# Kernel optimization log

Hardware: AMD Instinct MI355X
Metric: run time of the kernel (lower is better)

The kernel has to match this reference:

```python
import jax, jax.numpy as jnp
import numpy as np

H = 2048   # hidden_size
L = 512    # latent_dim
B, S = 4, 2048

def setup_inputs() -> dict:
    key = jax.random.key(0)
    ks = jax.random.split(key, 13)
    def lin(k, fan_in, shape):
        bound = 1.0 / np.sqrt(fan_in)
        return jax.random.uniform(k, shape, jnp.float32, -bound, bound)
    return {
        "hidden_states": jax.random.normal(ks[0], (B, S, H), jnp.float32),
        "num_reasoning_steps": 8,
        # to_latent: Linear(H, 2L) -> ReLU -> Linear(2L, L)
        "W_enc1": lin(ks[1], H, (2 * L, H)), "b_enc1": lin(ks[2], H, (2 * L,)),
        "W_enc2": lin(ks[3], 2 * L, (L, 2 * L)), "b_enc2": lin(ks[4], 2 * L, (L,)),
        # from_latent: Linear(L, 2L) -> ReLU -> Linear(2L, H)
        "W_dec1": lin(ks[5], L, (2 * L, L)), "b_dec1": lin(ks[6], L, (2 * L,)),
        "W_dec2": lin(ks[7], 2 * L, (H, 2 * L)), "b_dec2": lin(ks[8], 2 * L, (H,)),
        # GRUCell(L, L): weight_ih/hh [3L, L], bias_ih/hh [3L]
        "w_ih": lin(ks[9], L, (3 * L, L)), "w_hh": lin(ks[10], L, (3 * L, L)),
        "b_ih": lin(ks[11], L, (3 * L,)), "b_hh": lin(ks[12], L, (3 * L,)),
    }

def _gru_cell(x, h, w_ih, w_hh, b_ih, b_hh):
    # PyTorch GRUCell semantics
    gi = x @ w_ih.T + b_ih   # [*, 3L]
    gh = h @ w_hh.T + b_hh
    i_r, i_z, i_n = jnp.split(gi, 3, axis=-1)
    h_r, h_z, h_n = jnp.split(gh, 3, axis=-1)
    r = jax.nn.sigmoid(i_r + h_r)
    z = jax.nn.sigmoid(i_z + h_z)
    n = jnp.tanh(i_n + r * h_n)
    return (1.0 - z) * n + z * h

def reference(hidden_states, num_reasoning_steps, W_enc1, b_enc1, W_enc2, b_enc2,
              W_dec1, b_dec1, W_dec2, b_dec2, w_ih, w_hh, b_ih, b_hh):
    # encode to latent
    latent = jax.nn.relu(hidden_states @ W_enc1.T + b_enc1) @ W_enc2.T + b_enc2  # [B,S,L]

    def step(lat, _):
        lat = _gru_cell(lat, lat, w_ih, w_hh, b_ih, b_hh)
        return lat, lat

    latent, traj = jax.lax.scan(step, latent, None, length=num_reasoning_steps)
    # traj: [steps, B, S, L] -> [B, S, steps, L]
    latent_trajectory = jnp.transpose(traj, (1, 2, 0, 3))
    decoded = jax.nn.relu(latent @ W_dec1.T + b_dec1) @ W_dec2.T + b_dec2  # [B,S,H]
    return decoded, latent_trajectory
```

## Files before the change

### kernel.cpp

```cpp
#include <hip/hip_runtime.h>
#include <hip/hip_bf16.h>
#include <cstdint>
#include <cstddef>

#define TOKENS   8192
#define HID      2048
#define LAT      512
#define LAT2     1024
#define GCOLS    2048
#define STEPS    8
#define DEC_ELEMS (TOKENS*HID)

typedef __attribute__((ext_vector_type(8))) __bf16 bf16x8;
typedef __attribute__((ext_vector_type(4))) float  f32x4;
typedef __attribute__((ext_vector_type(8))) unsigned short u16x8;

__device__ __forceinline__ unsigned short f32_to_bf16_rne(float f) {
  unsigned int u = __float_as_uint(f);
  unsigned int r = (u + 0x7FFFu + ((u >> 16) & 1u)) >> 16;
  return (unsigned short)r;
}
__device__ __forceinline__ float bf16_to_f32(unsigned short u) {
  return __uint_as_float(((unsigned int)u) << 16);
}

__device__ __forceinline__ float sigmoidf_(float x) {
  if (x >= 0.f) { float e = __expf(-x); return 1.f / (1.f + e); }
  float e = __expf(x); return e / (1.f + e);
}
__device__ __forceinline__ float tanhf_(float x) {
  float ax = fabsf(x);
  float e  = __expf(-2.f * ax);
  float t  = (1.f - e) / (1.f + e);
  return copysignf(t, x);
}

__device__ __forceinline__ void gl_lds16(const void* g, void* l) {
  __builtin_amdgcn_global_load_lds(
      (const __attribute__((address_space(1))) void*)g,
      (__attribute__((address_space(3))) void*)l, 16, 0, 0);
}

__global__ void k_prep_w(const float* __restrict__ We1, const float* __restrict__ We2,
                         const float* __restrict__ Wd1, const float* __restrict__ Wd2,
                         unsigned short* __restrict__ We1b, unsigned short* __restrict__ We2b,
                         unsigned short* __restrict__ Wd1b, unsigned short* __restrict__ Wd2b) {
  const int total = 1310720;
  int i = blockIdx.x * blockDim.x + threadIdx.x;
  int stride = gridDim.x * blockDim.x;
  for (; i < total; i += stride) {
    const float* s; unsigned short* d; int j;
    if (i < 524288)       { s = We1; d = We1b; j = i; }
    else if (i < 655360)  { s = We2; d = We2b; j = i - 524288; }
    else if (i < 786432)  { s = Wd1; d = Wd1b; j = i - 655360; }
    else                  { s = Wd2; d = Wd2b; j = i - 786432; }
    float4 v = ((const float4*)s)[j];
    ushort4 o;
    o.x = f32_to_bf16_rne(v.x);
    o.y = f32_to_bf16_rne(v.y);
    o.z = f32_to_bf16_rne(v.z);
    o.w = f32_to_bf16_rne(v.w);
    ((ushort4*)d)[j] = o;
  }
}

__global__ void k_gru_pack(const float* __restrict__ wih, const float* __restrict__ whh,
                           const float* __restrict__ bih, const float* __restrict__ bhh,
                           unsigned short* __restrict__ Wg, float* __restrict__ biasg) {
  int gc = blockIdx.x;
  int l  = gc >> 2;
  int g  = gc & 3;
  int row = (g == 0) ? l : (g == 1) ? (512 + l) : (1024 + l);
  for (int c = threadIdx.x; c < LAT; c += blockDim.x) {
    float v;
    if (g <= 1)      v = wih[row * LAT + c] + whh[row * LAT + c];
    else if (g == 2) v = wih[row * LAT + c];
    else             v = whh[row * LAT + c];
    Wg[(size_t)gc * LAT + c] = f32_to_bf16_rne(v);
  }
  if (threadIdx.x == 0) {
    float b;
    if (g <= 1)      b = bih[row] + bhh[row];
    else if (g == 2) b = bih[row];
    else             b = bhh[row];
    biasg[gc] = b;
  }
}

#define MWG 128
#define NWG 128
#define KTILE 64

template <int EPI, int A32>
__global__ __launch_bounds__(256)
void gemm_bt(const void* __restrict__ Ap,
             const unsigned short* __restrict__ W,
             const float* __restrict__ bias,
             int K, int N,
             unsigned short* __restrict__ outB) {
  __shared__ __align__(16) char smem[2 * MWG * KTILE * 2];
  unsigned short* As = (unsigned short*)smem;
  unsigned short* Bs = As + MWG * KTILE;

  const int tid  = threadIdx.x;
  const int lane = tid & 63;
  const int wv   = tid >> 6;
  const int wr   = wv >> 1;
  const int wc   = wv & 1;
  const int m0   = blockIdx.x * MWG;
  const int n0   = blockIdx.y * NWG;

  const int lr = lane & 15;
  const int lq = lane >> 4;
  const int srow = lane >> 3;
  const int scol = (lane & 7) * 8;

  f32x4 acc[4][4];
#pragma unroll
  for (int i = 0; i < 4; ++i)
#pragma unroll
    for (int j = 0; j < 4; ++j) acc[i][j] = (f32x4){0.f, 0.f, 0.f, 0.f};

  const unsigned short* Ab = (const unsigned short*)Ap + (size_t)m0 * K;
  const float*          Af = (const float*)Ap + (size_t)m0 * K;
  const unsigned short* Wb = W + (size_t)n0 * K;

  const int KT = K / KTILE;
  for (int kt = 0; kt < KT; ++kt) {
    const int k0 = kt * KTILE;
#pragma unroll
    for (int q = 0; q < 4; ++q) {
      int row = 32 * wv + 8 * q + srow;
      if constexpr (!A32)
        gl_lds16(Ab + (size_t)row * K + k0 + scol, As + (32 * wv + 8 * q) * KTILE);
      gl_lds16(Wb + (size_t)row * K + k0 + scol, Bs + (32 * wv + 8 * q) * KTILE);
    }
    if constexpr (A32) {
#pragma unroll
      for (int q = 0; q < 4; ++q) {
        int row = 32 * wv + 8 * q + srow;
        const float* src = Af + (size_t)row * K + k0 + scol;
        float4 v0 = *(const float4*)src;
        float4 v1 = *(const float4*)(src + 4);
        u16x8 o;
        o[0] = f32_to_bf16_rne(v0.x); o[1] = f32_to_bf16_rne(v0.y);
        o[2] = f32_to_bf16_rne(v0.z); o[3] = f32_to_bf16_rne(v0.w);
        o[4] = f32_to_bf16_rne(v1.x); o[5] = f32_to_bf16_rne(v1.y);
        o[6] = f32_to_bf16_rne(v1.z); o[7] = f32_to_bf16_rne(v1.w);
        *(u16x8*)(As + (32 * wv + 8 * q) * KTILE + lane * 8) = o;
      }
    }
    __syncthreads();
#pragma unroll
    for (int kk = 0; kk < KTILE; kk += 32) {
      bf16x8 af[4], bf[4];
#pragma unroll
      for (int i = 0; i < 4; ++i)
        af[i] = *(const bf16x8*)(As + (wr * 64 + i * 16 + lr) * KTILE + kk + lq * 8);
#pragma unroll
      for (int j = 0; j < 4; ++j)
        bf[j] = *(const bf16x8*)(Bs + (wc * 64 + j * 16 + lr) * KTILE + kk + lq * 8);
#pragma unroll
      for (int i = 0; i < 4; ++i)
#pragma unroll
        for (int j = 0; j < 4; ++j)
          acc[i][j] = __builtin_amdgcn_mfma_f32_16x16x32_bf16(af[i], bf[j], acc[i][j], 0, 0, 0);
    }
    __syncthreads();
  }

  float bj[4];
#pragma unroll
  for (int j = 0; j < 4; ++j) bj[j] = bias[n0 + wc * 64 + j * 16 + lr];
#pragma unroll
  for (int i = 0; i < 4; ++i) {
#pragma unroll
    for (int ii = 0; ii < 4; ++ii) {
      int row = m0 + wr * 64 + i * 16 + 4 * lq + ii;
#pragma unroll
      for (int j = 0; j < 4; ++j) {
        int col = n0 + wc * 64 + j * 16 + lr;
        float v = acc[i][j][ii] + bj[j];
        if constexpr (EPI == 0) {
          outB[(size_t)row * N + col] = f32_to_bf16_rne(fmaxf(v, 0.f));
        } else {
          outB[(size_t)row * N + col] = f32_to_bf16_rne(v);
        }
      }
    }
  }
}


#define WAIT_LGKM0() asm volatile("s_waitcnt lgkmcnt(0)" ::: "memory")
#define WAIT_VM(n)   asm volatile("s_waitcnt vmcnt(" #n ")" ::: "memory")

#define LOAD_A(buf, mh) { \
  const int baseA = (buf)*65536 + wm*16384; \
  _Pragma("unroll") for (int m4 = 0; m4 < 4; ++m4) \
  _Pragma("unroll") for (int kki = 0; kki < 2; ++kki) { \
    int rl = (mh)*64 + m4*16 + lr; \
    int off = (rl*128 + kki*64 + lq*16) ^ ((rl & 7) << 4); \
    aR[mh][m4][kki] = *(const bf16x8*)(lds_ + baseA + off); } }

#define LOAD_B(buf, nh) { \
  const int baseB = (buf)*65536 + 32768 + (wn >> 1)*16384; \
  _Pragma("unroll") for (int n2 = 0; n2 < 2; ++n2) \
  _Pragma("unroll") for (int kki = 0; kki < 2; ++kki) { \
    int rl = (wn & 1)*64 + ((nh)*2 + n2)*16 + lr; \
    int off = (rl*128 + kki*64 + lq*16) ^ ((rl & 7) << 4); \
    bR[nh][n2][kki] = *(const bf16x8*)(lds_ + baseB + off); } }

#define STAGE_A(buf, half, kt) { \
  const unsigned short* gp = A + (size_t)(m0 + (half)*128 + rr8)*K + (size_t)(kt)*64 + cc8; \
  char* dp = lds_ + (buf)*65536 + (half)*16384 + (wv << 10); \
  gl_lds16(gp, dp); \
  gl_lds16(gp + (size_t)64*K, dp + 8192); }

#define STAGE_B(buf, half, kt) { \
  const unsigned short* gp = W + (size_t)(n0 + (half)*128 + rr8)*K + (size_t)(kt)*64 + cc8; \
  char* dp = lds_ + (buf)*65536 + 32768 + (half)*16384 + (wv << 10); \
  gl_lds16(gp, dp); \
  gl_lds16(gp + (size_t)64*K, dp + 8192); }

#define MFMAQ(mh, nh) \
  _Pragma("unroll") for (int kki = 0; kki < 2; ++kki) \
  _Pragma("unroll") for (int n2 = 0; n2 < 2; ++n2) \
  _Pragma("unroll") for (int m4 = 0; m4 < 4; ++m4) \
    acc[(mh)*4 + m4][(nh)*2 + n2] = __builtin_amdgcn_mfma_f32_16x16x32_bf16( \
        aR[mh][m4][kki], bR[nh][n2][kki], acc[(mh)*4 + m4][(nh)*2 + n2], 0, 0, 0);

#define PH_CORE(mh, nh) \
  __builtin_amdgcn_s_barrier(); \
  WAIT_LGKM0(); \
  __builtin_amdgcn_sched_barrier(0); \
  __builtin_amdgcn_s_setprio(1); \
  MFMAQ(mh, nh); \
  __builtin_amdgcn_sched_barrier(0); \
  __builtin_amdgcn_s_setprio(0);

#define PH_BAR() __builtin_amdgcn_s_barrier();

#define KLOOP_MAIN(tlim) \
  _Pragma("unroll 1") \
  for (int t = 0; t < (tlim); ++t) { \
    const int kt1 = 2 * t + 1, kt2 = 2 * t + 2, kt3 = 2 * t + 3; \
    LOAD_A(0, 0) LOAD_B(0, 0) \
    STAGE_A(1, 0, kt1) \
    PH_CORE(0, 0) PH_BAR() \
    LOAD_B(0, 1) \
    STAGE_A(1, 1, kt1) \
    PH_CORE(0, 1) PH_BAR() \
    LOAD_A(0, 1) \
    STAGE_B(0, 0, kt2) \
    PH_CORE(1, 1) PH_BAR() \
    STAGE_B(0, 1, kt2) \
    PH_CORE(1, 0) \
    WAIT_VM(4); \
    PH_BAR() \
    LOAD_A(1, 0) LOAD_B(1, 0) \
    STAGE_A(0, 0, kt2) \
    PH_CORE(0, 0) PH_BAR() \
    LOAD_B(1, 1) \
    STAGE_A(0, 1, kt2) \
    PH_CORE(0, 1) PH_BAR() \
    LOAD_A(1, 1) \
    STAGE_B(1, 0, kt3) \
    PH_CORE(1, 1) PH_BAR() \
    STAGE_B(1, 1, kt3) \
    PH_CORE(1, 0) \
    WAIT_VM(4); \
    PH_BAR() \
  }

#define KLOOP_LAST(ktL) { \
    LOAD_A(0, 0) LOAD_B(0, 0) \
    STAGE_A(1, 0, (ktL)) \
    PH_CORE(0, 0) PH_BAR() \
    LOAD_B(0, 1) \
    STAGE_A(1, 1, (ktL)) \
    PH_CORE(0, 1) PH_BAR() \
    LOAD_A(0, 1) \
    PH_CORE(1, 1) PH_BAR() \
    PH_CORE(1, 0) \
    WAIT_VM(0); \
    PH_BAR() \
    LOAD_A(1, 0) LOAD_B(1, 0) \
    PH_CORE(0, 0) PH_BAR() \
    LOAD_B(1, 1) \
    PH_CORE(0, 1) PH_BAR() \
    LOAD_A(1, 1) \
    PH_CORE(1, 1) PH_BAR() \
    PH_CORE(1, 0) \
    PH_BAR() \
  }

__global__ __launch_bounds__(512, 2)
void gemm256_f(const unsigned short* __restrict__ A,
               const unsigned short* __restrict__ W,
               const float* __restrict__ bias, int K, int N, int Ntiles,
               float* __restrict__ outF) {
  __shared__ __align__(16) char lds_[131072];

  const int tid  = threadIdx.x;
  const int lane = tid & 63;
  const int wv   = tid >> 6;
  const int wm   = wv >> 2;
  const int wn   = wv & 3;
  const int lr   = lane & 15;
  const int lq   = lane >> 4;
  const int rr8 = (wv << 3) + (lane >> 3);
  const int cc8 = ((lane & 7) ^ (lane >> 3)) << 3;

  const int nwg = gridDim.x;
  const int wg  = blockIdx.x;
  const int swz = (wg & 7) * (nwg >> 3) + (wg >> 3);
  const int tm  = swz / Ntiles;
  const int tn  = swz % Ntiles;
  const int m0  = tm * 256;
  const int n0  = tn * 256;

  f32x4 acc[8][4];
#pragma unroll
  for (int i = 0; i < 8; ++i)
#pragma unroll
    for (int j = 0; j < 4; ++j) acc[i][j] = (f32x4){0.f, 0.f, 0.f, 0.f};

  bf16x8 aR[2][4][2];
  bf16x8 bR[2][2][2];

  const int nIt = K >> 7;

  STAGE_B(0, 0, 0) STAGE_B(0, 1, 0) STAGE_A(0, 0, 0) STAGE_A(0, 1, 0)
  STAGE_B(1, 0, 1) STAGE_B(1, 1, 1)
  WAIT_VM(4);
  __builtin_amdgcn_s_barrier();

  KLOOP_MAIN(nIt - 1)
  KLOOP_LAST(2 * nIt - 1)

  float bj[4];
#pragma unroll
  for (int nf = 0; nf < 4; ++nf) bj[nf] = bias[n0 + wn * 64 + nf * 16 + lr];
#pragma unroll
  for (int mf = 0; mf < 8; ++mf) {
#pragma unroll
    for (int ii = 0; ii < 4; ++ii) {
      int row = m0 + wm * 128 + mf * 16 + lq * 4 + ii;
#pragma unroll
      for (int nf = 0; nf < 4; ++nf) {
        int col = n0 + wn * 64 + nf * 16 + lr;
        outF[(size_t)row * N + col] = acc[mf][nf][ii] + bj[nf];
      }
    }
  }
}

__global__ __launch_bounds__(512, 2)
void gemm256_gru(const unsigned short* __restrict__ A,
                 const unsigned short* __restrict__ W,
                 const float* __restrict__ bias,
                 int K, int N, int Ntiles,
                 unsigned short* __restrict__ outB,
                 const unsigned short* __restrict__ hInB,
                 float* __restrict__ traj,
                 int step) {
  __shared__ __align__(16) char lds_[131072];

  const int tid  = threadIdx.x;
  const int lane = tid & 63;
  const int wv   = tid >> 6;
  const int wm   = wv >> 2;
  const int wn   = wv & 3;
  const int lr   = lane & 15;
  const int lq   = lane >> 4;
  const int rr8 = (wv << 3) + (lane >> 3);
  const int cc8 = ((lane & 7) ^ (lane >> 3)) << 3;

  const int nwg = gridDim.x;
  const int wg  = blockIdx.x;
  const int swz = (wg & 7) * (nwg >> 3) + (wg >> 3);
  const int tm  = swz / Ntiles;
  const int tn  = swz % Ntiles;
  const int m0  = tm * 256;
  const int n0  = tn * 256;

  f32x4 acc[8][4];
#pragma unroll
  for (int i = 0; i < 8; ++i)
#pragma unroll
    for (int j = 0; j < 4; ++j) acc[i][j] = (f32x4){0.f, 0.f, 0.f, 0.f};

  bf16x8 aR[2][4][2];
  bf16x8 bR[2][2][2];

  const int nIt = K >> 7;

  STAGE_B(0, 0, 0) STAGE_B(0, 1, 0) STAGE_A(0, 0, 0) STAGE_A(0, 1, 0)
  STAGE_B(1, 0, 1) STAGE_B(1, 1, 1)
  WAIT_VM(4);
  __builtin_amdgcn_s_barrier();

  KLOOP_MAIN(nIt - 1)
  KLOOP_LAST(2 * nIt - 1)

  float bj[4];
#pragma unroll
  for (int nf = 0; nf < 4; ++nf) bj[nf] = bias[n0 + wn * 64 + nf * 16 + lr];

  float* scr = (float*)lds_ + wv * 1088;
  const int latBase = tn * 64 + wn * 16;
  const int la = lane & 15;
  const int th = lane >> 4;
#pragma unroll
  for (int mf = 0; mf < 8; ++mf) {
    WAIT_LGKM0();
#pragma unroll
    for (int nf = 0; nf < 4; ++nf)
#pragma unroll
      for (int ii = 0; ii < 4; ++ii)
        scr[(lq * 4 + ii) * 68 + nf * 16 + lr] = acc[mf][nf][ii] + bj[nf];
    WAIT_LGKM0();
#pragma unroll
    for (int tb = 0; tb < 4; ++tb) {
      int tt = th * 4 + tb;
      int token = m0 + wm * 128 + mf * 16 + tt;
      f32x4 g = *(const f32x4*)(scr + tt * 68 + la * 4);
      int latc = latBase + la;
      float h  = bf16_to_f32(hInB[(size_t)token * LAT + latc]);
      float r  = sigmoidf_(g.x);
      float z  = sigmoidf_(g.y);
      float n  = tanhf_(g.z + r * g.w);
      float hn = (1.f - z) * n + z * h;
      outB[(size_t)token * LAT + latc] = f32_to_bf16_rne(hn);
      traj[(size_t)token * (STEPS * LAT) + step * LAT + latc] = hn;
    }
  }
}

extern "C" void kernel_launch(void* const* d_in, const int* in_sizes, int n_in,
                              void* d_out, int out_size, void* d_ws, size_t ws_size,
                              hipStream_t stream) {
  const float* hs  = (const float*)d_in[0];
  const float* We1 = (const float*)d_in[2];
  const float* be1 = (const float*)d_in[3];
  const float* We2 = (const float*)d_in[4];
  const float* be2 = (const float*)d_in[5];
  const float* Wd1 = (const float*)d_in[6];
  const float* bd1 = (const float*)d_in[7];
  const float* Wd2 = (const float*)d_in[8];
  const float* bd2 = (const float*)d_in[9];
  const float* wih = (const float*)d_in[10];
  const float* whh = (const float*)d_in[11];
  const float* bih = (const float*)d_in[12];
  const float* bhh = (const float*)d_in[13];

  char* ws = (char*)d_ws;
  unsigned short* X2    = (unsigned short*)(ws + 0);
  unsigned short* We1b  = (unsigned short*)(ws + 33554432);
  unsigned short* We2b  = (unsigned short*)(ws + 37748736);
  unsigned short* Wd1b  = (unsigned short*)(ws + 38797312);
  unsigned short* Wd2b  = (unsigned short*)(ws + 39845888);
  unsigned short* Wg    = (unsigned short*)(ws + 44040192);
  float*          biasg = (float*)         (ws + 46137344);
  unsigned short* X1    = (unsigned short*)(ws + 46145536);
  unsigned short* Lb0   = (unsigned short*)(ws + 62922752);
  unsigned short* Lb1   = (unsigned short*)(ws + 71311360);

  float* dec  = (float*)d_out;
  float* traj = (float*)d_out + DEC_ELEMS;

  k_prep_w<<<1024, 256, 0, stream>>>(We1, We2, Wd1, Wd2, We1b, We2b, Wd1b, Wd2b);
  k_gru_pack<<<GCOLS, 128, 0, stream>>>(wih, whh, bih, bhh, Wg, biasg);

  gemm_bt<0, 1><<<dim3(TOKENS / MWG, LAT2 / NWG), dim3(256), 0, stream>>>(
      hs, We1b, be1, HID, LAT2, X1);
  gemm_bt<1, 0><<<dim3(TOKENS / MWG, LAT / NWG), dim3(256), 0, stream>>>(
      X1, We2b, be2, LAT2, LAT, Lb0);
  for (int s = 0; s < STEPS; ++s) {
    const unsigned short* lbi = (s & 1) ? Lb1 : Lb0;
    unsigned short*       lbo = (s & 1) ? Lb0 : Lb1;
    gemm256_gru<<<256, 512, 0, stream>>>(lbi, Wg, biasg, LAT, GCOLS, 8,
                                         lbo, lbi, traj, s);
  }
  gemm_bt<0, 0><<<dim3(TOKENS / MWG, LAT2 / NWG), dim3(256), 0, stream>>>(
      Lb0, Wd1b, bd1, LAT, LAT2, X2);
  gemm256_f<<<256, 512, 0, stream>>>(X2, Wd2b, bd2, LAT2, HID, 8, dec);
}
```

Baseline: 441.5 us.

## Run GRU steps on 128x128 gemm_bt tiles and merge weight-prep kernels

Replaces the 256x256 pipelined GRU GEMM with a new epilogue mode (EPI=2) of the simpler 128x128 gemm_bt kernel. This launches four times as many workgroups per step, spreading the short-K GEMM more evenly across CUs. The two weight-prep kernels are also merged into one launch to save a dispatch. The trade-off is that the GRU path loses the deeper LDS pipelining and the larger per-block data reuse of the 256-tile kernel.

Result: slower. 477.5 us (+8.2%).

```diff
diff --git a/kernel.cpp b/kernel.cpp
--- a/kernel.cpp
+++ b/kernel.cpp
@@ -41,49 +41,55 @@
       (__attribute__((address_space(3))) void*)l, 16, 0, 0);
 }
 
-__global__ void k_prep_w(const float* __restrict__ We1, const float* __restrict__ We2,
-                         const float* __restrict__ Wd1, const float* __restrict__ Wd2,
-                         unsigned short* __restrict__ We1b, unsigned short* __restrict__ We2b,
-                         unsigned short* __restrict__ Wd1b, unsigned short* __restrict__ Wd2b) {
-  const int total = 1310720;
-  int i = blockIdx.x * blockDim.x + threadIdx.x;
-  int stride = gridDim.x * blockDim.x;
-  for (; i < total; i += stride) {
-    const float* s; unsigned short* d; int j;
-    if (i < 524288)       { s = We1; d = We1b; j = i; }
-    else if (i < 655360)  { s = We2; d = We2b; j = i - 524288; }
-    else if (i < 786432)  { s = Wd1; d = Wd1b; j = i - 655360; }
-    else                  { s = Wd2; d = Wd2b; j = i - 786432; }
-    float4 v = ((const float4*)s)[j];
-    ushort4 o;
-    o.x = f32_to_bf16_rne(v.x);
-    o.y = f32_to_bf16_rne(v.y);
-    o.z = f32_to_bf16_rne(v.z);
-    o.w = f32_to_bf16_rne(v.w);
-    ((ushort4*)d)[j] = o;
-  }
-}
-
-__global__ void k_gru_pack(const float* __restrict__ wih, const float* __restrict__ whh,
-                           const float* __restrict__ bih, const float* __restrict__ bhh,
-                           unsigned short* __restrict__ Wg, float* __restrict__ biasg) {
-  int gc = blockIdx.x;
-  int l  = gc >> 2;
-  int g  = gc & 3;
-  int row = (g == 0) ? l : (g == 1) ? (512 + l) : (1024 + l);
-  for (int c = threadIdx.x; c < LAT; c += blockDim.x) {
-    float v;
-    if (g <= 1)      v = wih[row * LAT + c] + whh[row * LAT + c];
-    else if (g == 2) v = wih[row * LAT + c];
-    else             v = whh[row * LAT + c];
-    Wg[(size_t)gc * LAT + c] = f32_to_bf16_rne(v);
-  }
-  if (threadIdx.x == 0) {
-    float b;
-    if (g <= 1)      b = bih[row] + bhh[row];
-    else if (g == 2) b = bih[row];
-    else             b = bhh[row];
-    biasg[gc] = b;
+#define WAIT_LGKM0() asm volatile("s_waitcnt lgkmcnt(0)" ::: "memory")
+#define WAIT_VM(n)   asm volatile("s_waitcnt vmcnt(" #n ")" ::: "memory")
+
+__global__ __launch_bounds__(256)
+void k_prep_all(const float* __restrict__ We1, const float* __restrict__ We2,
+                const float* __restrict__ Wd1, const float* __restrict__ Wd2,
+                const float* __restrict__ wih, const float* __restrict__ whh,
+                const float* __restrict__ bih, const float* __restrict__ bhh,
+                unsigned short* __restrict__ We1b, unsigned short* __restrict__ We2b,
+                unsigned short* __restrict__ Wd1b, unsigned short* __restrict__ Wd2b,
+                unsigned short* __restrict__ Wg,   float* __restrict__ biasg) {
+  const int bid = blockIdx.x;
+  if (bid < 2048) {
+    int gc = bid;
+    int l  = gc >> 2;
+    int g  = gc & 3;
+    int row = (g == 0) ? l : (g == 1) ? (512 + l) : (1024 + l);
+    for (int c = threadIdx.x; c < LAT; c += blockDim.x) {
+      float v;
+      if (g <= 1)      v = wih[row * LAT + c] + whh[row * LAT + c];
+      else if (g == 2) v = wih[row * LAT + c];
+      else             v = whh[row * LAT + c];
+      Wg[(size_t)gc * LAT + c] = f32_to_bf16_rne(v);
+    }
+    if (threadIdx.x == 0) {
+      float b;
+      if (g <= 1)      b = bih[row] + bhh[row];
+      else if (g == 2) b = bih[row];
+      else             b = bhh[row];
+      biasg[gc] = b;
+    }
+  } else {
+    const int total = 1310720;
+    int i = (bid - 2048) * blockDim.x + threadIdx.x;
+    int stride = 256 * blockDim.x;
+    for (; i < total; i += stride) {
+      const float* s; unsigned short* d; int j;
+      if (i < 524288)       { s = We1; d = We1b; j = i; }
+      else if (i < 655360)  { s = We2; d = We2b; j = i - 524288; }
+      else if (i < 786432)  { s = Wd1; d = Wd1b; j = i - 655360; }
+      else                  { s = Wd2; d = Wd2b; j = i - 786432; }
+      float4 v = ((const float4*)s)[j];
+      ushort4 o;
+      o.x = f32_to_bf16_rne(v.x);
+      o.y = f32_to_bf16_rne(v.y);
+      o.z = f32_to_bf16_rne(v.z);
+      o.w = f32_to_bf16_rne(v.w);
+      ((ushort4*)d)[j] = o;
+    }
   }
 }
 
@@ -97,7 +103,10 @@
              const unsigned short* __restrict__ W,
              const float* __restrict__ bias,
              int K, int N,
-             unsigned short* __restrict__ outB) {
+             unsigned short* __restrict__ outB,
+             const unsigned short* __restrict__ hInB,
+             float* __restrict__ traj,
+             int step) {
   __shared__ __align__(16) char smem[2 * MWG * KTILE * 2];
   unsigned short* As = (unsigned short*)smem;
   unsigned short* Bs = As + MWG * KTILE;
@@ -172,28 +181,57 @@
   float bj[4];
 #pragma unroll
   for (int j = 0; j < 4; ++j) bj[j] = bias[n0 + wc * 64 + j * 16 + lr];
-#pragma unroll
-  for (int i = 0; i < 4; ++i) {
-#pragma unroll
-    for (int ii = 0; ii < 4; ++ii) {
-      int row = m0 + wr * 64 + i * 16 + 4 * lq + ii;
-#pragma unroll
-      for (int j = 0; j < 4; ++j) {
-        int col = n0 + wc * 64 + j * 16 + lr;
-        float v = acc[i][j][ii] + bj[j];
-        if constexpr (EPI == 0) {
-          outB[(size_t)row * N + col] = f32_to_bf16_rne(fmaxf(v, 0.f));
-        } else {
-          outB[(size_t)row * N + col] = f32_to_bf16_rne(v);
+
+  if constexpr (EPI == 0 || EPI == 1) {
+#pragma unroll
+    for (int i = 0; i < 4; ++i) {
+#pragma unroll
+      for (int ii = 0; ii < 4; ++ii) {
+        int row = m0 + wr * 64 + i * 16 + 4 * lq + ii;
+#pragma unroll
+        for (int j = 0; j < 4; ++j) {
+          int col = n0 + wc * 64 + j * 16 + lr;
+          float v = acc[i][j][ii] + bj[j];
+          if constexpr (EPI == 0) {
+            outB[(size_t)row * N + col] = f32_to_bf16_rne(fmaxf(v, 0.f));
+          } else {
+            outB[(size_t)row * N + col] = f32_to_bf16_rne(v);
+          }
         }
       }
     }
-  }
-}
-
-
-#define WAIT_LGKM0() asm volatile("s_waitcnt lgkmcnt(0)" ::: "memory")
-#define WAIT_VM(n)   asm volatile("s_waitcnt vmcnt(" #n ")" ::: "memory")
+  } else {
+    float* scr = (float*)smem + wv * 1088;
+    const int latBase = (n0 + wc * 64) >> 2;
+    const int la = lane & 15;
+    const int th = lane >> 4;
+#pragma unroll
+    for (int i = 0; i < 4; ++i) {
+      WAIT_LGKM0();
+#pragma unroll
+      for (int j = 0; j < 4; ++j)
+#pragma unroll
+        for (int ii = 0; ii < 4; ++ii)
+          scr[(lq * 4 + ii) * 68 + j * 16 + lr] = acc[i][j][ii] + bj[j];
+      WAIT_LGKM0();
+#pragma unroll
+      for (int tb = 0; tb < 4; ++tb) {
+        int tt = th * 4 + tb;
+        int token = m0 + wr * 64 + i * 16 + tt;
+        f32x4 g = *(const f32x4*)(scr + tt * 68 + la * 4);
+        int latc = latBase + la;
+        float h  = bf16_to_f32(hInB[(size_t)token * LAT + latc]);
+        float r  = sigmoidf_(g.x);
+        float z  = sigmoidf_(g.y);
+        float n  = tanhf_(g.z + r * g.w);
+        float hn = (1.f - z) * n + z * h;
+        outB[(size_t)token * LAT + latc] = f32_to_bf16_rne(hn);
+        traj[(size_t)token * (STEPS * LAT) + step * LAT + latc] = hn;
+      }
+    }
+  }
+}
+
 
 #define LOAD_A(buf, mh) { \
   const int baseA = (buf)*65536 + wm*16384; \
@@ -356,88 +394,6 @@
   }
 }
 
-__global__ __launch_bounds__(512, 2)
-void gemm256_gru(const unsigned short* __restrict__ A,
-                 const unsigned short* __restrict__ W,
-                 const float* __restrict__ bias,
-                 int K, int N, int Ntiles,
-                 unsigned short* __restrict__ outB,
-                 const unsigned short* __restrict__ hInB,
-                 float* __restrict__ traj,
-                 int step) {
-  __shared__ __align__(16) char lds_[131072];
-
-  const int tid  = threadIdx.x;
-  const int lane = tid & 63;
-  const int wv   = tid >> 6;
-  const int wm   = wv >> 2;
-  const int wn   = wv & 3;
-  const int lr   = lane & 15;
-  const int lq   = lane >> 4;
-  const int rr8 = (wv << 3) + (lane >> 3);
-  const int cc8 = ((lane & 7) ^ (lane >> 3)) << 3;
-
-  const int nwg = gridDim.x;
-  const int wg  = blockIdx.x;
-  const int swz = (wg & 7) * (nwg >> 3) + (wg >> 3);
-  const int tm  = swz / Ntiles;
-  const int tn  = swz % Ntiles;
-  const int m0  = tm * 256;
-  const int n0  = tn * 256;
-
-  f32x4 acc[8][4];
-#pragma unroll
-  for (int i = 0; i < 8; ++i)
-#pragma unroll
-    for (int j = 0; j < 4; ++j) acc[i][j] = (f32x4){0.f, 0.f, 0.f, 0.f};
-
-  bf16x8 aR[2][4][2];
-  bf16x8 bR[2][2][2];
-
-  const int nIt = K >> 7;
-
-  STAGE_B(0, 0, 0) STAGE_B(0, 1, 0) STAGE_A(0, 0, 0) STAGE_A(0, 1, 0)
-  STAGE_B(1, 0, 1) STAGE_B(1, 1, 1)
-  WAIT_VM(4);
-  __builtin_amdgcn_s_barrier();
-
-  KLOOP_MAIN(nIt - 1)
-  KLOOP_LAST(2 * nIt - 1)
-
-  float bj[4];
-#pragma unroll
-  for (int nf = 0; nf < 4; ++nf) bj[nf] = bias[n0 + wn * 64 + nf * 16 + lr];
-
-  float* scr = (float*)lds_ + wv * 1088;
-  const int latBase = tn * 64 + wn * 16;
-  const int la = lane & 15;
-  const int th = lane >> 4;
-#pragma unroll
-  for (int mf = 0; mf < 8; ++mf) {
-    WAIT_LGKM0();
-#pragma unroll
-    for (int nf = 0; nf < 4; ++nf)
-#pragma unroll
-      for (int ii = 0; ii < 4; ++ii)
-        scr[(lq * 4 + ii) * 68 + nf * 16 + lr] = acc[mf][nf][ii] + bj[nf];
-    WAIT_LGKM0();
-#pragma unroll
-    for (int tb = 0; tb < 4; ++tb) {
-      int tt = th * 4 + tb;
-      int token = m0 + wm * 128 + mf * 16 + tt;
-      f32x4 g = *(const f32x4*)(scr + tt * 68 + la * 4);
-      int latc = latBase + la;
-      float h  = bf16_to_f32(hInB[(size_t)token * LAT + latc]);
-      float r  = sigmoidf_(g.x);
-      float z  = sigmoidf_(g.y);
-      float n  = tanhf_(g.z + r * g.w);
-      float hn = (1.f - z) * n + z * h;
-      outB[(size_t)token * LAT + latc] = f32_to_bf16_rne(hn);
-      traj[(size_t)token * (STEPS * LAT) + step * LAT + latc] = hn;
-    }
-  }
-}
-
 extern "C" void kernel_launch(void* const* d_in, const int* in_sizes, int n_in,
                               void* d_out, int out_size, void* d_ws, size_t ws_size,
                               hipStream_t stream) {
@@ -470,20 +426,20 @@
   float* dec  = (float*)d_out;
   float* traj = (float*)d_out + DEC_ELEMS;
 
-  k_prep_w<<<1024, 256, 0, stream>>>(We1, We2, Wd1, Wd2, We1b, We2b, Wd1b, Wd2b);
-  k_gru_pack<<<GCOLS, 128, 0, stream>>>(wih, whh, bih, bhh, Wg, biasg);
+  k_prep_all<<<2304, 256, 0, stream>>>(We1, We2, Wd1, Wd2, wih, whh, bih, bhh,
+                                       We1b, We2b, Wd1b, Wd2b, Wg, biasg);
 
   gemm_bt<0, 1><<<dim3(TOKENS / MWG, LAT2 / NWG), dim3(256), 0, stream>>>(
-      hs, We1b, be1, HID, LAT2, X1);
+      hs, We1b, be1, HID, LAT2, X1, nullptr, nullptr, 0);
   gemm_bt<1, 0><<<dim3(TOKENS / MWG, LAT / NWG), dim3(256), 0, stream>>>(
-      X1, We2b, be2, LAT2, LAT, Lb0);
+      X1, We2b, be2, LAT2, LAT, Lb0, nullptr, nullptr, 0);
   for (int s = 0; s < STEPS; ++s) {
     const unsigned short* lbi = (s & 1) ? Lb1 : Lb0;
     unsigned short*       lbo = (s & 1) ? Lb0 : Lb1;
-    gemm256_gru<<<256, 512, 0, stream>>>(lbi, Wg, biasg, LAT, GCOLS, 8,
-                                         lbo, lbi, traj, s);
+    gemm_bt<2, 0><<<dim3(TOKENS / MWG, GCOLS / NWG), dim3(256), 0, stream>>>(
+        lbi, Wg, biasg, LAT, GCOLS, lbo, lbi, traj, s);
   }
   gemm_bt<0, 0><<<dim3(TOKENS / MWG, LAT2 / NWG), dim3(256), 0, stream>>>(
-      Lb0, Wd1b, bd1, LAT, LAT2, X2);
+      Lb0, Wd1b, bd1, LAT, LAT2, X2, nullptr, nullptr, 0);
   gemm256_f<<<256, 512, 0, stream>>>(X2, Wd2b, bd2, LAT2, HID, 8, dec);
 }
```

## Fold GRU and decoder weight prep into first encoder GEMM as extra blocks

Applied to the files above, without the earlier changes.

Only the encoder weight conversion now runs before the first GEMM. The GRU weight packing and decoder weight conversion move into an extra row of blocks (blockIdx.y==8) inside the first encoder GEMM launch, so they overlap with the GEMM and one kernel launch goes away. The GRU pack is also vectorised to float4 loads. The trade-off is 64 extra blocks that compete with the GEMM for compute units and memory bandwidth, which could lengthen its tail.

Result: slower. 461.3 us (+4.5%).

```diff
diff --git a/kernel.cpp b/kernel.cpp
--- a/kernel.cpp
+++ b/kernel.cpp
@@ -41,19 +41,19 @@
       (__attribute__((address_space(3))) void*)l, 16, 0, 0);
 }
 
-__global__ void k_prep_w(const float* __restrict__ We1, const float* __restrict__ We2,
-                         const float* __restrict__ Wd1, const float* __restrict__ Wd2,
-                         unsigned short* __restrict__ We1b, unsigned short* __restrict__ We2b,
-                         unsigned short* __restrict__ Wd1b, unsigned short* __restrict__ Wd2b) {
-  const int total = 1310720;
+#define WAIT_LGKM0() asm volatile("s_waitcnt lgkmcnt(0)" ::: "memory")
+#define WAIT_VM(n)   asm volatile("s_waitcnt vmcnt(" #n ")" ::: "memory")
+
+__global__ __launch_bounds__(256)
+void k_prep_early(const float* __restrict__ We1, const float* __restrict__ We2,
+                  unsigned short* __restrict__ We1b, unsigned short* __restrict__ We2b) {
+  const int total = 655360;
   int i = blockIdx.x * blockDim.x + threadIdx.x;
   int stride = gridDim.x * blockDim.x;
   for (; i < total; i += stride) {
     const float* s; unsigned short* d; int j;
-    if (i < 524288)       { s = We1; d = We1b; j = i; }
-    else if (i < 655360)  { s = We2; d = We2b; j = i - 524288; }
-    else if (i < 786432)  { s = Wd1; d = Wd1b; j = i - 655360; }
-    else                  { s = Wd2; d = Wd2b; j = i - 786432; }
+    if (i < 524288) { s = We1; d = We1b; j = i; }
+    else            { s = We2; d = We2b; j = i - 524288; }
     float4 v = ((const float4*)s)[j];
     ushort4 o;
     o.x = f32_to_bf16_rne(v.x);
@@ -64,26 +64,48 @@
   }
 }
 
-__global__ void k_gru_pack(const float* __restrict__ wih, const float* __restrict__ whh,
-                           const float* __restrict__ bih, const float* __restrict__ bhh,
-                           unsigned short* __restrict__ Wg, float* __restrict__ biasg) {
-  int gc = blockIdx.x;
-  int l  = gc >> 2;
-  int g  = gc & 3;
-  int row = (g == 0) ? l : (g == 1) ? (512 + l) : (1024 + l);
-  for (int c = threadIdx.x; c < LAT; c += blockDim.x) {
-    float v;
-    if (g <= 1)      v = wih[row * LAT + c] + whh[row * LAT + c];
-    else if (g == 2) v = wih[row * LAT + c];
-    else             v = whh[row * LAT + c];
-    Wg[(size_t)gc * LAT + c] = f32_to_bf16_rne(v);
-  }
-  if (threadIdx.x == 0) {
-    float b;
-    if (g <= 1)      b = bih[row] + bhh[row];
-    else if (g == 2) b = bih[row];
-    else             b = bhh[row];
+__device__ void prep_tail(int bx, int tid,
+                          const float* __restrict__ wih, const float* __restrict__ whh,
+                          const float* __restrict__ bih, const float* __restrict__ bhh,
+                          const float* __restrict__ Wd1, const float* __restrict__ Wd2,
+                          unsigned short* __restrict__ Wg, float* __restrict__ biasg,
+                          unsigned short* __restrict__ Wd1b, unsigned short* __restrict__ Wd2b) {
+  const int gtid = bx * 256 + tid;
+  for (int i = gtid; i < 262144; i += 16384) {
+    int gc = i >> 7;
+    int c4 = (i & 127) << 2;
+    int l = gc >> 2, g = gc & 3;
+    int row = (g == 0) ? l : (g == 1) ? (512 + l) : (1024 + l);
+    float4 a = *(const float4*)(wih + (size_t)row * 512 + c4);
+    float4 b = *(const float4*)(whh + (size_t)row * 512 + c4);
+    float4 v;
+    if (g <= 1)      { v.x = a.x + b.x; v.y = a.y + b.y; v.z = a.z + b.z; v.w = a.w + b.w; }
+    else if (g == 2) v = a;
+    else             v = b;
+    ushort4 o;
+    o.x = f32_to_bf16_rne(v.x);
+    o.y = f32_to_bf16_rne(v.y);
+    o.z = f32_to_bf16_rne(v.z);
+    o.w = f32_to_bf16_rne(v.w);
+    *(ushort4*)(Wg + (size_t)gc * 512 + c4) = o;
+  }
+  for (int gc = gtid; gc < 2048; gc += 16384) {
+    int l = gc >> 2, g = gc & 3;
+    int row = (g == 0) ? l : (g == 1) ? (512 + l) : (1024 + l);
+    float b = (g <= 1) ? (bih[row] + bhh[row]) : (g == 2 ? bih[row] : bhh[row]);
     biasg[gc] = b;
+  }
+  for (int i = gtid; i < 655360; i += 16384) {
+    const float* s; unsigned short* d; int j;
+    if (i < 131072) { s = Wd1; d = Wd1b; j = i; }
+    else            { s = Wd2; d = Wd2b; j = i - 131072; }
+    float4 v = ((const float4*)s)[j];
+    ushort4 o;
+    o.x = f32_to_bf16_rne(v.x);
+    o.y = f32_to_bf16_rne(v.y);
+    o.z = f32_to_bf16_rne(v.z);
+    o.w = f32_to_bf16_rne(v.w);
+    ((ushort4*)d)[j] = o;
   }
 }
 
@@ -91,13 +113,26 @@
 #define NWG 128
 #define KTILE 64
 
-template <int EPI, int A32>
+template <int EPI, int A32, int PREP>
 __global__ __launch_bounds__(256)
 void gemm_bt(const void* __restrict__ Ap,
              const unsigned short* __restrict__ W,
              const float* __restrict__ bias,
              int K, int N,
-             unsigned short* __restrict__ outB) {
+             unsigned short* __restrict__ outB,
+             const float* __restrict__ p_wih, const float* __restrict__ p_whh,
+             const float* __restrict__ p_bih, const float* __restrict__ p_bhh,
+             const float* __restrict__ p_Wd1, const float* __restrict__ p_Wd2,
+             unsigned short* __restrict__ p_Wg, float* __restrict__ p_biasg,
+             unsigned short* __restrict__ p_Wd1b, unsigned short* __restrict__ p_Wd2b) {
+  if constexpr (PREP) {
+    if (blockIdx.y == 8) {
+      prep_tail(blockIdx.x, threadIdx.x, p_wih, p_whh, p_bih, p_bhh,
+                p_Wd1, p_Wd2, p_Wg, p_biasg, p_Wd1b, p_Wd2b);
+      return;
+    }
+  }
+
   __shared__ __align__(16) char smem[2 * MWG * KTILE * 2];
   unsigned short* As = (unsigned short*)smem;
   unsigned short* Bs = As + MWG * KTILE;
@@ -191,9 +226,6 @@
   }
 }
 
-
-#define WAIT_LGKM0() asm volatile("s_waitcnt lgkmcnt(0)" ::: "memory")
-#define WAIT_VM(n)   asm volatile("s_waitcnt vmcnt(" #n ")" ::: "memory")
 
 #define LOAD_A(buf, mh) { \
   const int baseA = (buf)*65536 + wm*16384; \
@@ -470,20 +502,22 @@
   float* dec  = (float*)d_out;
   float* traj = (float*)d_out + DEC_ELEMS;
 
-  k_prep_w<<<1024, 256, 0, stream>>>(We1, We2, Wd1, Wd2, We1b, We2b, Wd1b, Wd2b);
-  k_gru_pack<<<GCOLS, 128, 0, stream>>>(wih, whh, bih, bhh, Wg, biasg);
-
-  gemm_bt<0, 1><<<dim3(TOKENS / MWG, LAT2 / NWG), dim3(256), 0, stream>>>(
-      hs, We1b, be1, HID, LAT2, X1);
-  gemm_bt<1, 0><<<dim3(TOKENS / MWG, LAT / NWG), dim3(256), 0, stream>>>(
-      X1, We2b, be2, LAT2, LAT, Lb0);
+  k_prep_early<<<1024, 256, 0, stream>>>(We1, We2, We1b, We2b);
+
+  gemm_bt<0, 1, 1><<<dim3(TOKENS / MWG, 9), dim3(256), 0, stream>>>(
+      hs, We1b, be1, HID, LAT2, X1,
+      wih, whh, bih, bhh, Wd1, Wd2, Wg, biasg, Wd1b, Wd2b);
+  gemm_bt<1, 0, 0><<<dim3(TOKENS / MWG, LAT / NWG), dim3(256), 0, stream>>>(
+      X1, We2b, be2, LAT2, LAT, Lb0,
+      nullptr, nullptr, nullptr, nullptr, nullptr, nullptr, nullptr, nullptr, nullptr, nullptr);
   for (int s = 0; s < STEPS; ++s) {
     const unsigned short* lbi = (s & 1) ? Lb1 : Lb0;
     unsigned short*       lbo = (s & 1) ? Lb0 : Lb1;
     gemm256_gru<<<256, 512, 0, stream>>>(lbi, Wg, biasg, LAT, GCOLS, 8,
                                          lbo, lbi, traj, s);
   }
-  gemm_bt<0, 0><<<dim3(TOKENS / MWG, LAT2 / NWG), dim3(256), 0, stream>>>(
-      Lb0, Wd1b, bd1, LAT, LAT2, X2);
+  gemm_bt<0, 0, 0><<<dim3(TOKENS / MWG, LAT2 / NWG), dim3(256), 0, stream>>>(
+      Lb0, Wd1b, bd1, LAT, LAT2, X2,
+      nullptr, nullptr, nullptr, nullptr, nullptr, nullptr, nullptr, nullptr, nullptr, nullptr);
   gemm256_f<<<256, 512, 0, stream>>>(X2, Wd2b, bd2, LAT2, HID, 8, dec);
 }
```

## Route encoder/decoder GEMMs through pipelined 256-tile kernel and fuse prep kernels

Applied to the files above, without the earlier changes.

Replaces the simple 128x128 gemm_bt kernel used for the two encoder GEMMs and the first decoder GEMM with the templated 256-tile pipelined gemm256 kernel, which gains bf16/ReLU epilogue variants. The fp32 hidden-state input is now converted to bf16 in a merged prep kernel that also converts the weights and packs the GRU weights. Previously that conversion happened inside the first GEMM's load path. This trades an extra 64MB read plus 32MB write for a faster main loop. The encoder GEMMs launch only 128 and 64 workgroups, which may underfill the GPU.

New measurement: 465.7 us. 5.5% more time.

```diff
diff --git a/kernel.cpp b/kernel.cpp
--- a/kernel.cpp
+++ b/kernel.cpp
@@ -13,7 +13,6 @@
 
 typedef __attribute__((ext_vector_type(8))) __bf16 bf16x8;
 typedef __attribute__((ext_vector_type(4))) float  f32x4;
-typedef __attribute__((ext_vector_type(8))) unsigned short u16x8;
 
 __device__ __forceinline__ unsigned short f32_to_bf16_rne(float f) {
   unsigned int u = __float_as_uint(f);
@@ -41,159 +40,64 @@
       (__attribute__((address_space(3))) void*)l, 16, 0, 0);
 }
 
-__global__ void k_prep_w(const float* __restrict__ We1, const float* __restrict__ We2,
-                         const float* __restrict__ Wd1, const float* __restrict__ Wd2,
-                         unsigned short* __restrict__ We1b, unsigned short* __restrict__ We2b,
-                         unsigned short* __restrict__ Wd1b, unsigned short* __restrict__ Wd2b) {
-  const int total = 1310720;
-  int i = blockIdx.x * blockDim.x + threadIdx.x;
-  int stride = gridDim.x * blockDim.x;
-  for (; i < total; i += stride) {
-    const float* s; unsigned short* d; int j;
-    if (i < 524288)       { s = We1; d = We1b; j = i; }
-    else if (i < 655360)  { s = We2; d = We2b; j = i - 524288; }
-    else if (i < 786432)  { s = Wd1; d = Wd1b; j = i - 655360; }
-    else                  { s = Wd2; d = Wd2b; j = i - 786432; }
-    float4 v = ((const float4*)s)[j];
-    ushort4 o;
-    o.x = f32_to_bf16_rne(v.x);
-    o.y = f32_to_bf16_rne(v.y);
-    o.z = f32_to_bf16_rne(v.z);
-    o.w = f32_to_bf16_rne(v.w);
-    ((ushort4*)d)[j] = o;
-  }
-}
-
-__global__ void k_gru_pack(const float* __restrict__ wih, const float* __restrict__ whh,
-                           const float* __restrict__ bih, const float* __restrict__ bhh,
-                           unsigned short* __restrict__ Wg, float* __restrict__ biasg) {
-  int gc = blockIdx.x;
-  int l  = gc >> 2;
-  int g  = gc & 3;
-  int row = (g == 0) ? l : (g == 1) ? (512 + l) : (1024 + l);
-  for (int c = threadIdx.x; c < LAT; c += blockDim.x) {
-    float v;
-    if (g <= 1)      v = wih[row * LAT + c] + whh[row * LAT + c];
-    else if (g == 2) v = wih[row * LAT + c];
-    else             v = whh[row * LAT + c];
-    Wg[(size_t)gc * LAT + c] = f32_to_bf16_rne(v);
-  }
-  if (threadIdx.x == 0) {
-    float b;
-    if (g <= 1)      b = bih[row] + bhh[row];
-    else if (g == 2) b = bih[row];
-    else             b = bhh[row];
-    biasg[gc] = b;
-  }
-}
-
-#define MWG 128
-#define NWG 128
-#define KTILE 64
-
-template <int EPI, int A32>
-__global__ __launch_bounds__(256)
-void gemm_bt(const void* __restrict__ Ap,
-             const unsigned short* __restrict__ W,
-             const float* __restrict__ bias,
-             int K, int N,
-             unsigned short* __restrict__ outB) {
-  __shared__ __align__(16) char smem[2 * MWG * KTILE * 2];
-  unsigned short* As = (unsigned short*)smem;
-  unsigned short* Bs = As + MWG * KTILE;
-
-  const int tid  = threadIdx.x;
-  const int lane = tid & 63;
-  const int wv   = tid >> 6;
-  const int wr   = wv >> 1;
-  const int wc   = wv & 1;
-  const int m0   = blockIdx.x * MWG;
-  const int n0   = blockIdx.y * NWG;
-
-  const int lr = lane & 15;
-  const int lq = lane >> 4;
-  const int srow = lane >> 3;
-  const int scol = (lane & 7) * 8;
-
-  f32x4 acc[4][4];
-#pragma unroll
-  for (int i = 0; i < 4; ++i)
-#pragma unroll
-    for (int j = 0; j < 4; ++j) acc[i][j] = (f32x4){0.f, 0.f, 0.f, 0.f};
-
-  const unsigned short* Ab = (const unsigned short*)Ap + (size_t)m0 * K;
-  const float*          Af = (const float*)Ap + (size_t)m0 * K;
-  const unsigned short* Wb = W + (size_t)n0 * K;
-
-  const int KT = K / KTILE;
-  for (int kt = 0; kt < KT; ++kt) {
-    const int k0 = kt * KTILE;
-#pragma unroll
-    for (int q = 0; q < 4; ++q) {
-      int row = 32 * wv + 8 * q + srow;
-      if constexpr (!A32)
-        gl_lds16(Ab + (size_t)row * K + k0 + scol, As + (32 * wv + 8 * q) * KTILE);
-      gl_lds16(Wb + (size_t)row * K + k0 + scol, Bs + (32 * wv + 8 * q) * KTILE);
-    }
-    if constexpr (A32) {
-#pragma unroll
-      for (int q = 0; q < 4; ++q) {
-        int row = 32 * wv + 8 * q + srow;
-        const float* src = Af + (size_t)row * K + k0 + scol;
-        float4 v0 = *(const float4*)src;
-        float4 v1 = *(const float4*)(src + 4);
-        u16x8 o;
-        o[0] = f32_to_bf16_rne(v0.x); o[1] = f32_to_bf16_rne(v0.y);
-        o[2] = f32_to_bf16_rne(v0.z); o[3] = f32_to_bf16_rne(v0.w);
-        o[4] = f32_to_bf16_rne(v1.x); o[5] = f32_to_bf16_rne(v1.y);
-        o[6] = f32_to_bf16_rne(v1.z); o[7] = f32_to_bf16_rne(v1.w);
-        *(u16x8*)(As + (32 * wv + 8 * q) * KTILE + lane * 8) = o;
-      }
-    }
-    __syncthreads();
-#pragma unroll
-    for (int kk = 0; kk < KTILE; kk += 32) {
-      bf16x8 af[4], bf[4];
-#pragma unroll
-      for (int i = 0; i < 4; ++i)
-        af[i] = *(const bf16x8*)(As + (wr * 64 + i * 16 + lr) * KTILE + kk + lq * 8);
-#pragma unroll
-      for (int j = 0; j < 4; ++j)
-        bf[j] = *(const bf16x8*)(Bs + (wc * 64 + j * 16 + lr) * KTILE + kk + lq * 8);
-#pragma unroll
-      for (int i = 0; i < 4; ++i)
-#pragma unroll
-        for (int j = 0; j < 4; ++j)
-          acc[i][j] = __builtin_amdgcn_mfma_f32_16x16x32_bf16(af[i], bf[j], acc[i][j], 0, 0, 0);
-    }
-    __syncthreads();
-  }
-
-  float bj[4];
-#pragma unroll
-  for (int j = 0; j < 4; ++j) bj[j] = bias[n0 + wc * 64 + j * 16 + lr];
-#pragma unroll
-  for (int i = 0; i < 4; ++i) {
-#pragma unroll
-    for (int ii = 0; ii < 4; ++ii) {
-      int row = m0 + wr * 64 + i * 16 + 4 * lq + ii;
-#pragma unroll
-      for (int j = 0; j < 4; ++j) {
-        int col = n0 + wc * 64 + j * 16 + lr;
-        float v = acc[i][j][ii] + bj[j];
-        if constexpr (EPI == 0) {
-          outB[(size_t)row * N + col] = f32_to_bf16_rne(fmaxf(v, 0.f));
-        } else {
-          outB[(size_t)row * N + col] = f32_to_bf16_rne(v);
-        }
-      }
-    }
-  }
-}
-
-
 #define WAIT_LGKM0() asm volatile("s_waitcnt lgkmcnt(0)" ::: "memory")
 #define WAIT_VM(n)   asm volatile("s_waitcnt vmcnt(" #n ")" ::: "memory")
+
+__global__ __launch_bounds__(256)
+void k_prep_all(const float* __restrict__ hs,
+                const float* __restrict__ We1, const float* __restrict__ We2,
+                const float* __restrict__ Wd1, const float* __restrict__ Wd2,
+                const float* __restrict__ wih, const float* __restrict__ whh,
+                const float* __restrict__ bih, const float* __restrict__ bhh,
+                unsigned short* __restrict__ A0,
+                unsigned short* __restrict__ We1b, unsigned short* __restrict__ We2b,
+                unsigned short* __restrict__ Wd1b, unsigned short* __restrict__ Wd2b,
+                unsigned short* __restrict__ Wg,   float* __restrict__ biasg) {
+  const int bid = blockIdx.x;
+  if (bid < 2048) {
+    int gc = bid;
+    int l  = gc >> 2;
+    int g  = gc & 3;
+    int row = (g == 0) ? l : (g == 1) ? (512 + l) : (1024 + l);
+    const float4* wa = (const float4*)(wih + (size_t)row * LAT);
+    const float4* wb = (const float4*)(whh + (size_t)row * LAT);
+    for (int c4 = threadIdx.x; c4 < 128; c4 += blockDim.x) {
+      float4 a = wa[c4], b = wb[c4], v;
+      if (g <= 1)      { v.x = a.x + b.x; v.y = a.y + b.y; v.z = a.z + b.z; v.w = a.w + b.w; }
+      else if (g == 2) v = a;
+      else             v = b;
+      ushort4 o;
+      o.x = f32_to_bf16_rne(v.x);
+      o.y = f32_to_bf16_rne(v.y);
+      o.z = f32_to_bf16_rne(v.z);
+      o.w = f32_to_bf16_rne(v.w);
+      ((ushort4*)(Wg + (size_t)gc * LAT))[c4] = o;
+    }
+    if (threadIdx.x == 0) {
+      biasg[gc] = (g <= 1) ? (bih[row] + bhh[row]) : (g == 2 ? bih[row] : bhh[row]);
+    }
+  } else {
+    const int total = 5505024;
+    int i = (bid - 2048) * 256 + threadIdx.x;
+    const int stride = 1024 * 256;
+    for (; i < total; i += stride) {
+      const float* s; unsigned short* d; int j;
+      if (i < 4194304)      { s = hs;  d = A0;   j = i; }
+      else if (i < 4718592) { s = We1; d = We1b; j = i - 4194304; }
+      else if (i < 4849664) { s = We2; d = We2b; j = i - 4718592; }
+      else if (i < 4980736) { s = Wd1; d = Wd1b; j = i - 4849664; }
+      else                  { s = Wd2; d = Wd2b; j = i - 4980736; }
+      float4 v = ((const float4*)s)[j];
+      ushort4 o;
+      o.x = f32_to_bf16_rne(v.x);
+      o.y = f32_to_bf16_rne(v.y);
+      o.z = f32_to_bf16_rne(v.z);
+      o.w = f32_to_bf16_rne(v.w);
+      ((ushort4*)d)[j] = o;
+    }
+  }
+}
+
 
 #define LOAD_A(buf, mh) { \
   const int baseA = (buf)*65536 + wm*16384; \
@@ -295,11 +199,14 @@
     PH_BAR() \
   }
 
+template <int EPI>
 __global__ __launch_bounds__(512, 2)
-void gemm256_f(const unsigned short* __restrict__ A,
-               const unsigned short* __restrict__ W,
-               const float* __restrict__ bias, int K, int N, int Ntiles,
-               float* __restrict__ outF) {
+void gemm256(const unsigned short* __restrict__ A,
+             const unsigned short* __restrict__ W,
+             const float* __restrict__ bias,
+             int K, int N, int Ntiles,
+             unsigned short* __restrict__ outB,
+             float* __restrict__ outF) {
   __shared__ __align__(16) char lds_[131072];
 
   const int tid  = threadIdx.x;
@@ -350,7 +257,14 @@
 #pragma unroll
       for (int nf = 0; nf < 4; ++nf) {
         int col = n0 + wn * 64 + nf * 16 + lr;
-        outF[(size_t)row * N + col] = acc[mf][nf][ii] + bj[nf];
+        float v = acc[mf][nf][ii] + bj[nf];
+        if constexpr (EPI == 0) {
+          outB[(size_t)row * N + col] = f32_to_bf16_rne(fmaxf(v, 0.f));
+        } else if constexpr (EPI == 1) {
+          outB[(size_t)row * N + col] = f32_to_bf16_rne(v);
+        } else {
+          outF[(size_t)row * N + col] = v;
+        }
       }
     }
   }
@@ -456,7 +370,7 @@
   const float* bhh = (const float*)d_in[13];
 
   char* ws = (char*)d_ws;
-  unsigned short* X2    = (unsigned short*)(ws + 0);
+  unsigned short* A0    = (unsigned short*)(ws + 0);
   unsigned short* We1b  = (unsigned short*)(ws + 33554432);
   unsigned short* We2b  = (unsigned short*)(ws + 37748736);
   unsigned short* Wd1b  = (unsigned short*)(ws + 38797312);
@@ -466,24 +380,23 @@
   unsigned short* X1    = (unsigned short*)(ws + 46145536);
   unsigned short* Lb0   = (unsigned short*)(ws + 62922752);
   unsigned short* Lb1   = (unsigned short*)(ws + 71311360);
+  unsigned short* X2    = A0;
 
   float* dec  = (float*)d_out;
   float* traj = (float*)d_out + DEC_ELEMS;
 
-  k_prep_w<<<1024, 256, 0, stream>>>(We1, We2, Wd1, Wd2, We1b, We2b, Wd1b, Wd2b);
-  k_gru_pack<<<GCOLS, 128, 0, stream>>>(wih, whh, bih, bhh, Wg, biasg);
-
-  gemm_bt<0, 1><<<dim3(TOKENS / MWG, LAT2 / NWG), dim3(256), 0, stream>>>(
-      hs, We1b, be1, HID, LAT2, X1);
-  gemm_bt<1, 0><<<dim3(TOKENS / MWG, LAT / NWG), dim3(256), 0, stream>>>(
-      X1, We2b, be2, LAT2, LAT, Lb0);
+  k_prep_all<<<3072, 256, 0, stream>>>(hs, We1, We2, Wd1, Wd2,
+                                       wih, whh, bih, bhh,
+                                       A0, We1b, We2b, Wd1b, Wd2b, Wg, biasg);
+
+  gemm256<0><<<128, 512, 0, stream>>>(A0, We1b, be1, HID, LAT2, 4, X1, nullptr);
+  gemm256<1><<<64,  512, 0, stream>>>(X1, We2b, be2, LAT2, LAT, 2, Lb0, nullptr);
   for (int s = 0; s < STEPS; ++s) {
     const unsigned short* lbi = (s & 1) ? Lb1 : Lb0;
     unsigned short*       lbo = (s & 1) ? Lb0 : Lb1;
     gemm256_gru<<<256, 512, 0, stream>>>(lbi, Wg, biasg, LAT, GCOLS, 8,
                                          lbo, lbi, traj, s);
   }
-  gemm_bt<0, 0><<<dim3(TOKENS / MWG, LAT2 / NWG), dim3(256), 0, stream>>>(
-      Lb0, Wd1b, bd1, LAT, LAT2, X2);
-  gemm256_f<<<256, 512, 0, stream>>>(X2, Wd2b, bd2, LAT2, HID, 8, dec);
-}
+  gemm256<0><<<128, 512, 0, stream>>>(Lb0, Wd1b, bd1, LAT, LAT2, 4, X2, nullptr);
+  gemm256<2><<<256, 512, 0, stream>>>(X2, Wd2b, bd2, LAT2, HID, 8, nullptr, dec);
+}
```
